# Performance work log

Measured on AMD Instinct MI355X. Metric: run time of the kernel, lower is better.

## Reference

```python
import jax, jax.numpy as jnp
import numpy as np

N_EMBED = 1024
N_HEADS = 16


def setup_inputs() -> dict:
    key = jax.random.key(0)
    k_x, k_wa, k_wp = jax.random.split(key, 3)
    B, T, C = 2, 2048, N_EMBED
    x = jax.random.normal(k_x, (B, T, C), dtype=jnp.float32)
    # flax Dense default: lecun_normal kernel, zero bias; use scaled normal here
    w_attn = jax.random.normal(k_wa, (C, 3 * C), dtype=jnp.float32) / np.sqrt(C)
    b_attn = jnp.zeros((3 * C,), dtype=jnp.float32)
    w_proj = jax.random.normal(k_wp, (C, C), dtype=jnp.float32) / np.sqrt(C)
    b_proj = jnp.zeros((C,), dtype=jnp.float32)
    return {"x": x, "w_attn": w_attn, "b_attn": b_attn,
            "w_proj": w_proj, "b_proj": b_proj}


def reference(x, w_attn, b_attn, w_proj, b_proj):
    B, T, C = x.shape
    H = N_HEADS
    D = C // H
    qkv = x @ w_attn + b_attn                      # [B,T,3C]
    q, k, v = jnp.split(qkv, 3, axis=-1)           # each [B,T,C]
    q = q.reshape(B, T, H, D).swapaxes(1, 2)       # [B,H,T,D]
    k = k.reshape(B, T, H, D).swapaxes(1, 2)
    v = v.reshape(B, T, H, D).swapaxes(1, 2)
    att = jnp.einsum('bhid,bhjd->bhij', q, k) * (1.0 / jnp.sqrt(D))
    causal = jnp.tril(jnp.ones((T, T), dtype=bool))
    att = jnp.where(causal, att, -jnp.inf)
    att = jax.nn.softmax(att, axis=-1)
    y = jnp.einsum('bhij,bhjd->bhid', att, v)      # [B,H,T,D]
    y = y.swapaxes(1, 2).reshape(B, T, C)
    return y @ w_proj + b_proj
```

## Files before the change

### kernel.cpp

```cpp
#include <hip/hip_runtime.h>
#include <hip/hip_bf16.h>

typedef __bf16 bf16x8 __attribute__((ext_vector_type(8)));
typedef float f32x4 __attribute__((ext_vector_type(4)));
typedef float f32x16 __attribute__((ext_vector_type(16)));
typedef unsigned short u16;
typedef unsigned int u32;
typedef u16 u16x8 __attribute__((ext_vector_type(8)));
typedef u32 u32x4 __attribute__((ext_vector_type(4)));

#define SM_SCALE 0.1803368801111244f

#define FEXP2(x) __builtin_amdgcn_exp2f(x)

__device__ inline u16 tobf(float f) {
  u32 u = __builtin_bit_cast(u32, f);
  u32 r = (u + 0x7fffu + ((u >> 16) & 1u)) >> 16;
  return (u16)r;
}

__device__ inline void gload_lds16(const void* g, void* lds) {
  __builtin_amdgcn_global_load_lds(
      (const __attribute__((address_space(1))) u32*)g,
      (__attribute__((address_space(3))) u32*)lds, 16, 0, 0);
}

template <int N>
__device__ __forceinline__ void wait_vmcnt() {
  if constexpr (N == 0)
    asm volatile("s_waitcnt vmcnt(0)" ::: "memory");
  else if constexpr (N == 5)
    asm volatile("s_waitcnt vmcnt(5)" ::: "memory");
  else if constexpr (N == 7)
    asm volatile("s_waitcnt vmcnt(7)" ::: "memory");
}

__device__ __forceinline__ void transpose_body(const float* __restrict__ in,
                                               u16* __restrict__ out, int K,
                                               int N, int bxg, int tid) {
  __shared__ float tile[32][33];
  int nbx = N >> 5;
  int bx = bxg % nbx, by = bxg / nbx;
  int k0 = by << 5, n0 = bx << 5;
  int tx = tid & 31, ty = tid >> 5;
#pragma unroll
  for (int j = 0; j < 4; ++j) {
    int row = ty + j * 8;
    tile[row][tx] = in[(size_t)(k0 + row) * N + n0 + tx];
  }
  __syncthreads();
#pragma unroll
  for (int j = 0; j < 4; ++j) {
    int row = ty + j * 8;
    out[(size_t)(n0 + row) * K + k0 + tx] = tobf(tile[tx][row]);
  }
}

__global__ __launch_bounds__(256) void prep_kernel(
    const float* __restrict__ x, u16* __restrict__ xb,
    const float* __restrict__ wa, u16* __restrict__ wat,
    const float* __restrict__ wp, u16* __restrict__ wpt) {
  const int b = blockIdx.x, tid = threadIdx.x;
  if (b < 2048) {
    int i = b * 256 + tid;
    const float4* p = (const float4*)x + (size_t)i * 2;
    float4 a = p[0], c = p[1];
    u16x8 v;
    v[0] = tobf(a.x); v[1] = tobf(a.y); v[2] = tobf(a.z); v[3] = tobf(a.w);
    v[4] = tobf(c.x); v[5] = tobf(c.y); v[6] = tobf(c.z); v[7] = tobf(c.w);
    *(u16x8*)(xb + (size_t)i * 8) = v;
  } else if (b < 5120) {
    transpose_body(wa, wat, 1024, 3072, b - 2048, tid);
  } else {
    transpose_body(wp, wpt, 1024, 1024, b - 5120, tid);
  }
}

template <int EPI, int BN>
__global__ __launch_bounds__(256) void gemm_bt(
    const u16* __restrict__ A, const u16* __restrict__ Bt,
    const float* __restrict__ bias,
    u16* __restrict__ o0, u16* __restrict__ o1, u16* __restrict__ o2,
    float* __restrict__ fo, int M, int N, int K) {
  constexpr int NF = BN / 32;
  __shared__ __align__(16) u16 As[2][128 * 64];
  __shared__ __align__(16) u16 Bs[2][BN * 64];
  const int tid = threadIdx.x;
  const int lane = tid & 63;
  const int wave = tid >> 6;
  const int nbn = N / BN;
  int bid = (int)blockIdx.x;
  const int cpx = (int)gridDim.x >> 3;
  bid = (bid & 7) * cpx + (bid >> 3);
  const int bm = bid / nbn, bn = bid % nbn;
  const int m0 = bm << 7, n0 = bn * BN;
  const int wr = wave >> 1, wc = wave & 1;
  const int r15 = lane & 15, g = lane >> 4;

  f32x4 acc[4][NF] = {};

#define GSTAGE(buf, kt)                                                    \
  do {                                                                     \
    _Pragma("unroll")                                                      \
    for (int j = 0; j < 4; ++j) {                                          \
      int c = j * 4 + wave;                                                \
      int byte0 = c * 1024 + lane * 16;                                    \
      int row = byte0 >> 7;                                                \
      int colb = (byte0 & 127) ^ ((row & 7) << 4);                         \
      gload_lds16(A + (size_t)(m0 + row) * K + (kt) * 64 + (colb >> 1),    \
                  (char*)As[(buf)] + c * 1024);                            \
    }                                                                      \
    _Pragma("unroll")                                                      \
    for (int j = 0; j < NF; ++j) {                                         \
      int c = j * 4 + wave;                                                \
      int byte0 = c * 1024 + lane * 16;                                    \
      int row = byte0 >> 7;                                                \
      int colb = (byte0 & 127) ^ ((row & 7) << 4);                         \
      gload_lds16(Bt + (size_t)(n0 + row) * K + (kt) * 64 + (colb >> 1),   \
                  (char*)Bs[(buf)] + c * 1024);                            \
    }                                                                      \
  } while (0)

  const int nkt = K >> 6;
  GSTAGE(0, 0);
  for (int kt = 0; kt < nkt; ++kt) {
    const int cur = kt & 1;
    if (kt + 1 < nkt) {
      GSTAGE(cur ^ 1, kt + 1);
      wait_vmcnt<4 + NF>();
    } else {
      wait_vmcnt<0>();
    }
    __builtin_amdgcn_s_barrier();
#pragma unroll
    for (int kk = 0; kk < 2; ++kk) {
      bf16x8 af[4], bf[NF];
#pragma unroll
      for (int i = 0; i < 4; ++i) {
        int rowA = wr * 64 + i * 16 + r15;
        int ca = (kk * 64 + 16 * g) ^ ((rowA & 7) << 4);
        af[i] = *(const bf16x8*)((const char*)As[cur] + rowA * 128 + ca);
      }
#pragma unroll
      for (int j2 = 0; j2 < NF; ++j2) {
        int rowB = wc * (BN / 2) + j2 * 16 + r15;
        int cb = (kk * 64 + 16 * g) ^ ((rowB & 7) << 4);
        bf[j2] = *(const bf16x8*)((const char*)Bs[cur] + rowB * 128 + cb);
      }
#pragma unroll
      for (int i = 0; i < 4; ++i)
#pragma unroll
        for (int j2 = 0; j2 < NF; ++j2)
          acc[i][j2] = __builtin_amdgcn_mfma_f32_16x16x32_bf16(
              af[i], bf[j2], acc[i][j2], 0, 0, 0);
    }
    if (kt + 1 < nkt) __builtin_amdgcn_s_barrier();
  }
#undef GSTAGE

#pragma unroll
  for (int j2 = 0; j2 < NF; ++j2) {
    const int n = n0 + wc * (BN / 2) + j2 * 16 + r15;
    const float bv = bias[n];
#pragma unroll
    for (int i = 0; i < 4; ++i) {
      const int mb = m0 + wr * 64 + i * 16 + g * 4;
      float v[4];
#pragma unroll
      for (int rr = 0; rr < 4; ++rr) v[rr] = acc[i][j2][rr] + bv;
      if (EPI == 1) {
#pragma unroll
        for (int rr = 0; rr < 4; ++rr) fo[(size_t)(mb + rr) * N + n] = v[rr];
      } else {
        const int b = mb >> 11, t = mb & 2047;
        const int sec = n >> 10, nn = n & 1023;
        const int h = nn >> 6, d = nn & 63;
        const int bh = b * 16 + h;
        if (sec == 0) {
          u16* base = o0 + ((size_t)bh * 2048 + t) * 64 + d;
#pragma unroll
          for (int rr = 0; rr < 4; ++rr) base[rr * 64] = tobf(v[rr] * SM_SCALE);
        } else if (sec == 1) {
          u16* kb = o1 +
                    (((size_t)(bh * 32 + (t >> 6)) * 4 + (d >> 4)) * 2) * 512 +
                    ((d >> 3) & 1) * 256 + (d & 7);
          const int tb = t & 63;
#pragma unroll
          for (int rr = 0; rr < 4; ++rr) {
            int r = tb + rr;
            kb[(r >> 5) * 512 + (r & 31) * 8] = tobf(v[rr]);
          }
        } else {
          const int tl = t & 63;
          u16* vb = o2 +
                    ((((size_t)(bh * 32 + (t >> 6)) * 4 + (tl >> 4)) * 2 +
                      (d >> 5)) * 512) +
                    ((tl >> 3) & 1) * 256 + (d & 31) * 8 + (tl & 7);
          u32* p = (u32*)vb;
          p[0] = (u32)tobf(v[0]) | ((u32)tobf(v[1]) << 16);
          p[1] = (u32)tobf(v[2]) | ((u32)tobf(v[3]) << 16);
        }
      }
    }
  }
}

__global__ __launch_bounds__(256) void attn_kernel(
    const u16* __restrict__ qb, const u16* __restrict__ kpk,
    const u16* __restrict__ vpk, u16* __restrict__ yb) {
  __shared__ float Of[4][32 * 67];
  __shared__ float Ml[4][32], Ll[4][32];
  const int tid = threadIdx.x;
  const int lane = tid & 63;
  const int kw = tid >> 6;
  const int q31 = lane & 31, hi = lane >> 5;
  const int bx = blockIdx.x;
  const int cq = 63 - (bx >> 5);
  const int bh = bx & 31;
  const int q0 = cq * 32;
  const int qg = q0 + q31;
  const int ktEnd = ((q0 + 31) >> 6) + 1;

  const u16* qrow = qb + ((size_t)bh * 2048 + qg) * 64;
  bf16x8 aq[4];
#pragma unroll
  for (int ks = 0; ks < 4; ++ks)
    aq[ks] = *(const bf16x8*)(qrow + ks * 16 + 8 * hi);

  f32x16 o0 = {}, o1 = {};
  float m = -INFINITY, l = 0.f;

  const u16* kbh = kpk + (size_t)bh * 32 * 4096 + lane * 8;
  const u16* vbh = vpk + (size_t)bh * 32 * 4096 + lane * 8;

  for (int kt = kw; kt < ktEnd; kt += 4) {
    const u16* kp = kbh + (size_t)kt * 4096;
    const u16* vp = vbh + (size_t)kt * 4096;

    bf16x8 kf[8];
#pragma unroll
    for (int j = 0; j < 8; ++j) kf[j] = *(const bf16x8*)(kp + j * 512);

    f32x16 s0 = {}, s1 = {};
    __builtin_amdgcn_s_setprio(1);
#pragma unroll
    for (int ks = 0; ks < 4; ++ks) {
      s0 = __builtin_amdgcn_mfma_f32_32x32x16_bf16(kf[2 * ks], aq[ks], s0, 0, 0, 0);
      s1 = __builtin_amdgcn_mfma_f32_32x32x16_bf16(kf[2 * ks + 1], aq[ks], s1, 0, 0, 0);
    }
    __builtin_amdgcn_s_setprio(0);

    if (kt * 64 + 63 > q0) {
      const int thr = qg - kt * 64;
#pragma unroll
      for (int r = 0; r < 16; ++r) {
        const int off = (r & 3) + 8 * (r >> 2) + 4 * hi;
        if (off > thr) s0[r] = -INFINITY;
        if (off + 32 > thr) s1[r] = -INFINITY;
      }
    }
    f32x16 mx;
#pragma unroll
    for (int r = 0; r < 16; ++r) mx[r] = fmaxf(s0[r], s1[r]);
#pragma unroll
    for (int st = 8; st >= 1; st >>= 1)
#pragma unroll
      for (int r = 0; r < st; ++r) mx[r] = fmaxf(mx[r], mx[r + st]);
    float mt = fmaxf(mx[0], __shfl_xor(mx[0], 32, 64));

    if (kt == kw) {
      m = mt;
    } else if (__any(mt > m + 8.f)) {
      float mnew = fmaxf(m, mt);
      float alpha = FEXP2(m - mnew);
      m = mnew;
      l *= alpha;
#pragma unroll
      for (int r = 0; r < 16; ++r) {
        o0[r] *= alpha;
        o1[r] *= alpha;
      }
    }
#pragma unroll
    for (int r = 0; r < 16; ++r) {
      s0[r] = FEXP2(s0[r] - m);
      s1[r] = FEXP2(s1[r] - m);
    }
    {
      float la = 0.f, lb = 0.f, lc2 = 0.f, ld = 0.f;
#pragma unroll
      for (int r = 0; r < 16; r += 2) {
        la += s0[r];
        lb += s0[r + 1];
        lc2 += s1[r];
        ld += s1[r + 1];
      }
      l += (la + lb) + (lc2 + ld);
    }
    u32 W[16];
#pragma unroll
    for (int i2 = 0; i2 < 8; ++i2) {
      asm("v_cvt_pk_bf16_f32 %0, %1, %2"
          : "=v"(W[i2]) : "v"(s0[2 * i2]), "v"(s0[2 * i2 + 1]));
      asm("v_cvt_pk_bf16_f32 %0, %1, %2"
          : "=v"(W[8 + i2]) : "v"(s1[2 * i2]), "v"(s1[2 * i2 + 1]));
    }
#pragma unroll
    for (int b4 = 0; b4 < 16; b4 += 4) {
      asm("v_permlane32_swap_b32 %0, %1" : "+v"(W[b4]), "+v"(W[b4 + 2]));
      asm("v_permlane32_swap_b32 %0, %1" : "+v"(W[b4 + 1]), "+v"(W[b4 + 3]));
    }
    bf16x8 vf[8];
#pragma unroll
    for (int j = 0; j < 8; ++j) vf[j] = *(const bf16x8*)(vp + j * 512);

    __builtin_amdgcn_s_setprio(1);
#pragma unroll
    for (int ks = 0; ks < 4; ++ks) {
      u32x4 pwv = {W[4 * ks], W[4 * ks + 1], W[4 * ks + 2], W[4 * ks + 3]};
      bf16x8 pf = __builtin_bit_cast(bf16x8, pwv);
      o0 = __builtin_amdgcn_mfma_f32_32x32x16_bf16(vf[2 * ks], pf, o0, 0, 0, 0);
      o1 = __builtin_amdgcn_mfma_f32_32x32x16_bf16(vf[2 * ks + 1], pf, o1, 0, 0, 0);
    }
    __builtin_amdgcn_s_setprio(0);
  }

  l += __shfl_xor(l, 32, 64);

  float* OfW = &Of[kw][0];
#pragma unroll
  for (int r = 0; r < 16; ++r) {
    const int d = (r & 3) + 8 * (r >> 2) + 4 * hi;
    OfW[q31 * 67 + d] = o0[r];
    OfW[q31 * 67 + d + 32] = o1[r];
  }
  if (hi == 0) {
    Ml[kw][q31] = m;
    Ll[kw][q31] = l;
  }
  __syncthreads();

  const int q = tid >> 3, d0 = (tid & 7) * 8;
  const float m0 = Ml[0][q], m1 = Ml[1][q], m2 = Ml[2][q], m3 = Ml[3][q];
  const float Mx = fmaxf(fmaxf(m0, m1), fmaxf(m2, m3));
  const float w0 = FEXP2(m0 - Mx), w1 = FEXP2(m1 - Mx);
  const float w2 = FEXP2(m2 - Mx), w3 = FEXP2(m3 - Mx);
  const float L = w0 * Ll[0][q] + w1 * Ll[1][q] + w2 * Ll[2][q] + w3 * Ll[3][q];
  const float inv = 1.0f / L;
  const int b = bh >> 4, hd = bh & 15;
  u32* dst = (u32*)(yb + ((size_t)b * 2048 + q0 + q) * 1024 + hd * 64 + d0);
  const int base = q * 67 + d0;
#pragma unroll
  for (int e = 0; e < 8; e += 2) {
    float v0 = (Of[0][base + e] * w0 + Of[1][base + e] * w1 +
                Of[2][base + e] * w2 + Of[3][base + e] * w3) * inv;
    float v1 = (Of[0][base + e + 1] * w0 + Of[1][base + e + 1] * w1 +
                Of[2][base + e + 1] * w2 + Of[3][base + e + 1] * w3) * inv;
    dst[e >> 1] = (u32)tobf(v0) | ((u32)tobf(v1) << 16);
  }
}

extern "C" void kernel_launch(void* const* d_in, const int* in_sizes, int n_in,
                              void* d_out, int out_size, void* d_ws,
                              size_t ws_size, hipStream_t stream) {
  const float* x = (const float*)d_in[0];
  const float* w_attn = (const float*)d_in[1];
  const float* b_attn = (const float*)d_in[2];
  const float* w_proj = (const float*)d_in[3];
  const float* b_proj = (const float*)d_in[4];
  float* out = (float*)d_out;
  char* ws = (char*)d_ws;

  u16* xb = (u16*)ws;
  u16* wat = (u16*)(ws + (8ull << 20));
  u16* wpt = (u16*)(ws + (14ull << 20));
  u16* qbuf = (u16*)(ws + (16ull << 20));
  u16* kpk = (u16*)(ws + (24ull << 20));
  u16* vpk = (u16*)(ws + (32ull << 20));
  u16* yb = (u16*)(ws + (40ull << 20));

  prep_kernel<<<6144, 256, 0, stream>>>(x, xb, w_attn, wat, w_proj, wpt);
  gemm_bt<0, 192><<<32 * 16, 256, 0, stream>>>(xb, wat, b_attn, qbuf, kpk,
                                               vpk, nullptr, 4096, 3072, 1024);
  attn_kernel<<<2048, 256, 0, stream>>>(qbuf, kpk, vpk, yb);
  gemm_bt<1, 64><<<32 * 16, 256, 0, stream>>>(yb, wpt, b_proj, nullptr,
                                              nullptr, nullptr, out, 4096,
                                              1024, 1024);
}
```

Before: 97.96 us.

## Cut attention kernel registers and LDS: split K/V loads, bf16 partial merge

Splits the K and V fragment loads into half-size groups interleaved with the MFMAs, and converts P to bf16 in four small groups just before each PV MFMA pair. The goal is lower peak VGPR pressure, and launch bounds now request 5 waves per SIMD. The cross-wave merge now stores each wave's partial output already normalized, in bf16 packed pairs, together with a log-sum-exp weight. This roughly halves the LDS footprint, which raises occupancy and cuts LDS traffic. The cost is an extra bf16 rounding of the partial outputs and a possible spill risk under the tighter register bound.

```diff
diff --git a/kernel.cpp b/kernel.cpp
--- a/kernel.cpp
+++ b/kernel.cpp
@@ -12,11 +12,16 @@
 #define SM_SCALE 0.1803368801111244f
 
 #define FEXP2(x) __builtin_amdgcn_exp2f(x)
+#define FLOG2(x) __builtin_amdgcn_logf(x)
 
 __device__ inline u16 tobf(float f) {
   u32 u = __builtin_bit_cast(u32, f);
   u32 r = (u + 0x7fffu + ((u >> 16) & 1u)) >> 16;
   return (u16)r;
+}
+
+__device__ inline float frombf(u16 h) {
+  return __builtin_bit_cast(float, (u32)h << 16);
 }
 
 __device__ inline void gload_lds16(const void* g, void* lds) {
@@ -205,11 +210,11 @@
   }
 }
 
-__global__ __launch_bounds__(256) void attn_kernel(
+__global__ __launch_bounds__(256, 5) void attn_kernel(
     const u16* __restrict__ qb, const u16* __restrict__ kpk,
     const u16* __restrict__ vpk, u16* __restrict__ yb) {
-  __shared__ float Of[4][32 * 67];
-  __shared__ float Ml[4][32], Ll[4][32];
+  __shared__ u32 OfU[4 * 1056];
+  __shared__ float Mw[4][32];
   const int tid = threadIdx.x;
   const int lane = tid & 63;
   const int kw = tid >> 6;
@@ -237,18 +242,36 @@
     const u16* kp = kbh + (size_t)kt * 4096;
     const u16* vp = vbh + (size_t)kt * 4096;
 
-    bf16x8 kf[8];
-#pragma unroll
-    for (int j = 0; j < 8; ++j) kf[j] = *(const bf16x8*)(kp + j * 512);
-
     f32x16 s0 = {}, s1 = {};
-    __builtin_amdgcn_s_setprio(1);
-#pragma unroll
-    for (int ks = 0; ks < 4; ++ks) {
-      s0 = __builtin_amdgcn_mfma_f32_32x32x16_bf16(kf[2 * ks], aq[ks], s0, 0, 0, 0);
-      s1 = __builtin_amdgcn_mfma_f32_32x32x16_bf16(kf[2 * ks + 1], aq[ks], s1, 0, 0, 0);
-    }
-    __builtin_amdgcn_s_setprio(0);
+    {
+      bf16x8 k0 = *(const bf16x8*)(kp);
+      bf16x8 k1 = *(const bf16x8*)(kp + 512);
+      bf16x8 k2 = *(const bf16x8*)(kp + 1024);
+      bf16x8 k3 = *(const bf16x8*)(kp + 1536);
+      __builtin_amdgcn_s_setprio(1);
+      s0 = __builtin_amdgcn_mfma_f32_32x32x16_bf16(k0, aq[0], s0, 0, 0, 0);
+      s1 = __builtin_amdgcn_mfma_f32_32x32x16_bf16(k1, aq[0], s1, 0, 0, 0);
+      s0 = __builtin_amdgcn_mfma_f32_32x32x16_bf16(k2, aq[1], s0, 0, 0, 0);
+      s1 = __builtin_amdgcn_mfma_f32_32x32x16_bf16(k3, aq[1], s1, 0, 0, 0);
+      __builtin_amdgcn_s_setprio(0);
+    }
+    {
+      bf16x8 k0 = *(const bf16x8*)(kp + 2048);
+      bf16x8 k1 = *(const bf16x8*)(kp + 2560);
+      bf16x8 k2 = *(const bf16x8*)(kp + 3072);
+      bf16x8 k3 = *(const bf16x8*)(kp + 3584);
+      __builtin_amdgcn_s_setprio(1);
+      s0 = __builtin_amdgcn_mfma_f32_32x32x16_bf16(k0, aq[2], s0, 0, 0, 0);
+      s1 = __builtin_amdgcn_mfma_f32_32x32x16_bf16(k1, aq[2], s1, 0, 0, 0);
+      s0 = __builtin_amdgcn_mfma_f32_32x32x16_bf16(k2, aq[3], s0, 0, 0, 0);
+      s1 = __builtin_amdgcn_mfma_f32_32x32x16_bf16(k3, aq[3], s1, 0, 0, 0);
+      __builtin_amdgcn_s_setprio(0);
+    }
+
+    bf16x8 vfA0 = *(const bf16x8*)(vp);
+    bf16x8 vfA1 = *(const bf16x8*)(vp + 512);
+    bf16x8 vfA2 = *(const bf16x8*)(vp + 1024);
+    bf16x8 vfA3 = *(const bf16x8*)(vp + 1536);
 
     if (kt * 64 + 63 > q0) {
       const int thr = qg - kt * 64;
@@ -297,66 +320,81 @@
       }
       l += (la + lb) + (lc2 + ld);
     }
-    u32 W[16];
-#pragma unroll
-    for (int i2 = 0; i2 < 8; ++i2) {
-      asm("v_cvt_pk_bf16_f32 %0, %1, %2"
-          : "=v"(W[i2]) : "v"(s0[2 * i2]), "v"(s0[2 * i2 + 1]));
-      asm("v_cvt_pk_bf16_f32 %0, %1, %2"
-          : "=v"(W[8 + i2]) : "v"(s1[2 * i2]), "v"(s1[2 * i2 + 1]));
-    }
-#pragma unroll
-    for (int b4 = 0; b4 < 16; b4 += 4) {
-      asm("v_permlane32_swap_b32 %0, %1" : "+v"(W[b4]), "+v"(W[b4 + 2]));
-      asm("v_permlane32_swap_b32 %0, %1" : "+v"(W[b4 + 1]), "+v"(W[b4 + 3]));
-    }
-    bf16x8 vf[8];
-#pragma unroll
-    for (int j = 0; j < 8; ++j) vf[j] = *(const bf16x8*)(vp + j * 512);
-
-    __builtin_amdgcn_s_setprio(1);
-#pragma unroll
-    for (int ks = 0; ks < 4; ++ks) {
-      u32x4 pwv = {W[4 * ks], W[4 * ks + 1], W[4 * ks + 2], W[4 * ks + 3]};
-      bf16x8 pf = __builtin_bit_cast(bf16x8, pwv);
-      o0 = __builtin_amdgcn_mfma_f32_32x32x16_bf16(vf[2 * ks], pf, o0, 0, 0, 0);
-      o1 = __builtin_amdgcn_mfma_f32_32x32x16_bf16(vf[2 * ks + 1], pf, o1, 0, 0, 0);
-    }
-    __builtin_amdgcn_s_setprio(0);
+    bf16x8 vfB0 = *(const bf16x8*)(vp + 2048);
+    bf16x8 vfB1 = *(const bf16x8*)(vp + 2560);
+    bf16x8 vfB2 = *(const bf16x8*)(vp + 3072);
+    bf16x8 vfB3 = *(const bf16x8*)(vp + 3584);
+
+#define PVG(SV, BASE, VA, VB)                                              \
+  do {                                                                     \
+    u32 Wk0, Wk1, Wk2, Wk3;                                                \
+    asm("v_cvt_pk_bf16_f32 %0, %1, %2"                                     \
+        : "=v"(Wk0) : "v"(SV[(BASE) + 0]), "v"(SV[(BASE) + 1]));           \
+    asm("v_cvt_pk_bf16_f32 %0, %1, %2"                                     \
+        : "=v"(Wk1) : "v"(SV[(BASE) + 2]), "v"(SV[(BASE) + 3]));           \
+    asm("v_cvt_pk_bf16_f32 %0, %1, %2"                                     \
+        : "=v"(Wk2) : "v"(SV[(BASE) + 4]), "v"(SV[(BASE) + 5]));           \
+    asm("v_cvt_pk_bf16_f32 %0, %1, %2"                                     \
+        : "=v"(Wk3) : "v"(SV[(BASE) + 6]), "v"(SV[(BASE) + 7]));           \
+    asm("v_permlane32_swap_b32 %0, %1" : "+v"(Wk0), "+v"(Wk2));            \
+    asm("v_permlane32_swap_b32 %0, %1" : "+v"(Wk1), "+v"(Wk3));            \
+    u32x4 pwv = {Wk0, Wk1, Wk2, Wk3};                                      \
+    bf16x8 pf = __builtin_bit_cast(bf16x8, pwv);                           \
+    __builtin_amdgcn_s_setprio(1);                                         \
+    o0 = __builtin_amdgcn_mfma_f32_32x32x16_bf16(VA, pf, o0, 0, 0, 0);     \
+    o1 = __builtin_amdgcn_mfma_f32_32x32x16_bf16(VB, pf, o1, 0, 0, 0);     \
+    __builtin_amdgcn_s_setprio(0);                                         \
+  } while (0)
+
+    PVG(s0, 0, vfA0, vfA1);
+    PVG(s0, 8, vfA2, vfA3);
+    PVG(s1, 0, vfB0, vfB1);
+    PVG(s1, 8, vfB2, vfB3);
+#undef PVG
   }
 
   l += __shfl_xor(l, 32, 64);
 
-  float* OfW = &Of[kw][0];
-#pragma unroll
-  for (int r = 0; r < 16; ++r) {
+  float invl, MwV;
+  if (l > 0.f) {
+    invl = 1.0f / l;
+    MwV = m + FLOG2(l);
+  } else {
+    invl = 0.f;
+    MwV = -INFINITY;
+  }
+  u32* OfW = OfU + kw * 1056 + q31 * 33;
+#pragma unroll
+  for (int r = 0; r < 16; r += 2) {
     const int d = (r & 3) + 8 * (r >> 2) + 4 * hi;
-    OfW[q31 * 67 + d] = o0[r];
-    OfW[q31 * 67 + d + 32] = o1[r];
-  }
-  if (hi == 0) {
-    Ml[kw][q31] = m;
-    Ll[kw][q31] = l;
-  }
+    OfW[d >> 1] =
+        (u32)tobf(o0[r] * invl) | ((u32)tobf(o0[r + 1] * invl) << 16);
+    OfW[(d + 32) >> 1] =
+        (u32)tobf(o1[r] * invl) | ((u32)tobf(o1[r + 1] * invl) << 16);
+  }
+  if (hi == 0) Mw[kw][q31] = MwV;
   __syncthreads();
 
-  const int q = tid >> 3, d0 = (tid & 7) * 8;
-  const float m0 = Ml[0][q], m1 = Ml[1][q], m2 = Ml[2][q], m3 = Ml[3][q];
-  const float Mx = fmaxf(fmaxf(m0, m1), fmaxf(m2, m3));
-  const float w0 = FEXP2(m0 - Mx), w1 = FEXP2(m1 - Mx);
-  const float w2 = FEXP2(m2 - Mx), w3 = FEXP2(m3 - Mx);
-  const float L = w0 * Ll[0][q] + w1 * Ll[1][q] + w2 * Ll[2][q] + w3 * Ll[3][q];
-  const float inv = 1.0f / L;
+  const int q = tid >> 3, c0 = (tid & 7) * 4;
+  const float m0v = Mw[0][q], m1v = Mw[1][q], m2v = Mw[2][q], m3v = Mw[3][q];
+  const float Mx = fmaxf(fmaxf(m0v, m1v), fmaxf(m2v, m3v));
+  const float w0 = FEXP2(m0v - Mx), w1 = FEXP2(m1v - Mx);
+  const float w2 = FEXP2(m2v - Mx), w3 = FEXP2(m3v - Mx);
+  const float invW = 1.0f / (w0 + w1 + w2 + w3);
   const int b = bh >> 4, hd = bh & 15;
-  u32* dst = (u32*)(yb + ((size_t)b * 2048 + q0 + q) * 1024 + hd * 64 + d0);
-  const int base = q * 67 + d0;
-#pragma unroll
-  for (int e = 0; e < 8; e += 2) {
-    float v0 = (Of[0][base + e] * w0 + Of[1][base + e] * w1 +
-                Of[2][base + e] * w2 + Of[3][base + e] * w3) * inv;
-    float v1 = (Of[0][base + e + 1] * w0 + Of[1][base + e + 1] * w1 +
-                Of[2][base + e + 1] * w2 + Of[3][base + e + 1] * w3) * inv;
-    dst[e >> 1] = (u32)tobf(v0) | ((u32)tobf(v1) << 16);
+  u32* dst = (u32*)(yb + ((size_t)b * 2048 + q0 + q) * 1024 + hd * 64) + c0;
+  const int base = q * 33 + c0;
+#pragma unroll
+  for (int cc = 0; cc < 4; ++cc) {
+    const u32 v0 = OfU[0 * 1056 + base + cc];
+    const u32 v1 = OfU[1 * 1056 + base + cc];
+    const u32 v2 = OfU[2 * 1056 + base + cc];
+    const u32 v3 = OfU[3 * 1056 + base + cc];
+    float lo = frombf((u16)v0) * w0 + frombf((u16)v1) * w1 +
+               frombf((u16)v2) * w2 + frombf((u16)v3) * w3;
+    float hi2 = frombf((u16)(v0 >> 16)) * w0 + frombf((u16)(v1 >> 16)) * w1 +
+                frombf((u16)(v2 >> 16)) * w2 + frombf((u16)(v3 >> 16)) * w3;
+    dst[cc] = (u32)tobf(lo * invW) | ((u32)tobf(hi2 * invW) << 16);
   }
 }
 
```

Result: slower. 154.7 us (+58.0%).
